# Kernel optimization log

Hardware: AMD Instinct MI355X
Metric: run time of the kernel (lower is better)

## Reference

```python
import jax, jax.numpy as jnp
import numpy as np

N_NODES = 100000
N_EDGES = 1600000
IN_F = 64
OUT_F = 40
K_HOPS = 3
N_CLUSTERS = 10000


def setup_inputs() -> dict:
    key = jax.random.key(0)
    k1, k2, k3, k4 = jax.random.split(key, 4)
    x = jax.random.normal(k1, (N_NODES, IN_F), dtype=jnp.float32)
    edge_index = jax.random.randint(k2, (2, N_EDGES), 0, N_NODES, dtype=jnp.int32)
    cluster_index = jax.random.randint(k3, (N_NODES,), 0, N_CLUSTERS, dtype=jnp.int32)
    W = jax.random.normal(k4, (OUT_F, IN_F), dtype=jnp.float32) * (1.0 / np.sqrt(IN_F))
    b = jnp.zeros((OUT_F,), dtype=jnp.float32)
    return {"x": x, "edge_index": edge_index, "cluster_index": cluster_index,
            "num_clusters": N_CLUSTERS, "W": W, "b": b}


def reference(x, edge_index, cluster_index, num_clusters, W, b):
    N = x.shape[0]
    self_loop = jnp.arange(N, dtype=edge_index.dtype)
    row = jnp.concatenate([edge_index[0], self_loop])  # target nodes
    col = jnp.concatenate([edge_index[1], self_loop])  # source nodes
    ones = jnp.ones(row.shape[0], dtype=x.dtype)
    deg = jax.ops.segment_sum(ones, row, num_segments=N)
    dinv = jax.lax.rsqrt(jnp.maximum(deg, 1.0))
    norm = dinv[row] * dinv[col]  # [E+N] symmetric GCN normalization
    # K-hop propagation: x <- D^{-1/2} (A+I) D^{-1/2} x, K times
    for _ in range(K_HOPS):
        x = jax.ops.segment_sum(x[col] * norm[:, None], row, num_segments=N)
    # cluster/compress: segment-mean of node features per cluster -> [C, F]
    cnt = jax.ops.segment_sum(jnp.ones(N, dtype=x.dtype), cluster_index,
                              num_segments=num_clusters)
    xc = jax.ops.segment_sum(x, cluster_index, num_segments=num_clusters)
    xc = xc / jnp.maximum(cnt, 1.0)[:, None]
    # dense linear on compressed rows, then reconstruct (gather back)
    h = xc @ W.T + b  # [C, OUT_F]
    out = h[cluster_index]  # [N, OUT_F]
    # original module computes log_softmax into a local `out` but returns x
    return out
```

## Files before the change

### kernel.cpp

```cpp
#include <hip/hip_runtime.h>

#define N_NODES    100000
#define N_EDGES    1600000
#define IN_F       64
#define OUT_F      40
#define N_CLUSTERS 10000

#define BUCK_SHIFT 7
#define BROWS      128
#define NBUCK      ((N_NODES + BROWS - 1) >> BUCK_SHIFT)
#define CAP        2560
#define TILE_E     4096
#define EPT        (TILE_E / 256)

typedef _Float16 half_t;
typedef _Float16 half4_t __attribute__((ext_vector_type(4)));

__global__ __launch_bounds__(256) void bin_scatter_kernel(
        const int* __restrict__ rows, const int* __restrict__ cols,
        int* __restrict__ bcursor, unsigned* __restrict__ bins) {
    __shared__ uint2 se[TILE_E];
    __shared__ int lh[NBUCK];
    __shared__ int lsc[NBUCK];
    __shared__ int lb[NBUCK];
    __shared__ int sc[256];
    int t = threadIdx.x;
    for (int i = t; i < NBUCK; i += 256) lh[i] = 0;
    __syncthreads();
    int e0 = blockIdx.x * TILE_E;
    int r[EPT], c[EPT], rk[EPT];
    #pragma unroll
    for (int k = 0; k < EPT; ++k) {
        int e = e0 + t + k * 256;
        if (e < N_EDGES) {
            r[k] = rows[e]; c[k] = cols[e];
            rk[k] = atomicAdd(&lh[r[k] >> BUCK_SHIFT], 1);
        } else r[k] = -1;
    }
    __syncthreads();
    int b4 = t * 4;
    int a0 = (b4 + 0 < NBUCK) ? lh[b4 + 0] : 0;
    int a1 = (b4 + 1 < NBUCK) ? lh[b4 + 1] : 0;
    int a2 = (b4 + 2 < NBUCK) ? lh[b4 + 2] : 0;
    int a3 = (b4 + 3 < NBUCK) ? lh[b4 + 3] : 0;
    int thr = a0 + a1 + a2 + a3;
    sc[t] = thr;
    __syncthreads();
    for (int off = 1; off < 256; off <<= 1) {
        int a = (t >= off) ? sc[t - off] : 0;
        __syncthreads();
        sc[t] += a;
        __syncthreads();
    }
    int ex = sc[t] - thr;
    if (b4 + 0 < NBUCK) { lsc[b4 + 0] = ex;                lb[b4 + 0] = a0 ? atomicAdd(&bcursor[b4 + 0], a0) : 0; }
    if (b4 + 1 < NBUCK) { lsc[b4 + 1] = ex + a0;           lb[b4 + 1] = a1 ? atomicAdd(&bcursor[b4 + 1], a1) : 0; }
    if (b4 + 2 < NBUCK) { lsc[b4 + 2] = ex + a0 + a1;      lb[b4 + 2] = a2 ? atomicAdd(&bcursor[b4 + 2], a2) : 0; }
    if (b4 + 3 < NBUCK) { lsc[b4 + 3] = ex + a0 + a1 + a2; lb[b4 + 3] = a3 ? atomicAdd(&bcursor[b4 + 3], a3) : 0; }
    __syncthreads();
    #pragma unroll
    for (int k = 0; k < EPT; ++k) {
        if (r[k] >= 0) {
            int bu = r[k] >> BUCK_SHIFT;
            se[lsc[bu] + rk[k]] = make_uint2((unsigned)r[k], (unsigned)c[k]);
        }
    }
    __syncthreads();
    #pragma unroll
    for (int k = 0; k < EPT; ++k) {
        int idx = k * 256 + t;
        if (e0 + idx < N_EDGES) {
            uint2 u = se[idx];
            int bu = (int)(u.x >> BUCK_SHIFT);
            int pos = lb[bu] + (idx - lsc[bu]);
            if (pos < CAP)
                bins[(size_t)bu * CAP + pos] = ((u.x & (BROWS - 1)) << 17) | u.y;
        }
    }
}

__global__ __launch_bounds__(256) void csr_build_kernel(
        const unsigned* __restrict__ bins, const int* __restrict__ bcnt,
        int* __restrict__ csr_col, uint2* __restrict__ rowinfo,
        float* __restrict__ dinv, const int* __restrict__ cl,
        int* __restrict__ ccnt) {
    __shared__ int lcnt[BROWS];
    __shared__ int gbeg[BROWS];
    __shared__ int sc[BROWS];
    int b = blockIdx.x, t = threadIdx.x;
    int n = min(bcnt[b], CAP);
    const unsigned* eb = bins + (size_t)b * CAP;
    if (t < BROWS) lcnt[t] = 0;
    __syncthreads();
    for (int i = t; i < n; i += 256) atomicAdd(&lcnt[eb[i] >> 17], 1);
    __syncthreads();
    int v = (t < BROWS) ? lcnt[t] : 0;
    if (t < BROWS) sc[t] = v;
    __syncthreads();
    for (int off = 1; off < BROWS; off <<= 1) {
        int a = (t >= off && t < BROWS) ? sc[t - off] : 0;
        __syncthreads();
        if (t < BROWS) sc[t] += a;
        __syncthreads();
    }
    if (t < BROWS) {
        int beg = b * CAP + sc[t] - v;
        gbeg[t] = beg;
        int grow = (b << BUCK_SHIFT) + t;
        if (grow < N_NODES) {
            rowinfo[grow] = make_uint2((unsigned)beg, (unsigned)v);
            dinv[grow] = rsqrtf((float)(v + 1));
            atomicAdd(&ccnt[cl[grow]], 1);
        }
        lcnt[t] = 0;
    }
    __syncthreads();
    for (int i = t; i < n; i += 256) {
        unsigned u = eb[i];
        int lrow = (int)(u >> 17);
        int pos = atomicAdd(&lcnt[lrow], 1);
        csr_col[gbeg[lrow] + pos] = (int)(u & 0x1FFFFu);
    }
}

__global__ __launch_bounds__(256) void prologue_kernel(
        const float4* __restrict__ x4, const float* __restrict__ W,
        const float* __restrict__ dinv, half_t* __restrict__ z0) {
    __shared__ float Ws[OUT_F * 68];
    int t = threadIdx.x;
    for (int i = t; i < OUT_F * IN_F; i += 256)
        Ws[(i >> 6) * 68 + (i & 63)] = W[i];
    __syncthreads();
    int node = blockIdx.x * 256 + t;
    if (node >= N_NODES) return;
    float4 xr[16];
    const float4* xp = x4 + (size_t)node * 16;
    #pragma unroll
    for (int k = 0; k < 16; ++k) xr[k] = xp[k];
    float d = dinv[node];
    half4_t* zp = (half4_t*)(z0 + (size_t)node * OUT_F);
    #pragma unroll
    for (int oq = 0; oq < 10; ++oq) {
        half4_t h;
        #pragma unroll
        for (int c = 0; c < 4; ++c) {
            const float4* wr = (const float4*)(Ws + (oq * 4 + c) * 68);
            float acc = 0.f;
            #pragma unroll
            for (int k = 0; k < 16; ++k) {
                float4 wv = wr[k];
                acc += xr[k].x * wv.x + xr[k].y * wv.y
                     + xr[k].z * wv.z + xr[k].w * wv.w;
            }
            h[c] = (half_t)(acc * d);
        }
        zp[oq] = h;
    }
}

template<int FINAL>
__global__ __launch_bounds__(256, 8) void hop40_kernel(
        const half_t* __restrict__ zin, half_t* __restrict__ zout,
        const uint2* __restrict__ rowinfo, const int* __restrict__ csr_col,
        const float* __restrict__ dinv, const int* __restrict__ cl,
        float* __restrict__ xc) {
    __shared__ half4_t srow[160];
    int t = threadIdx.x;
    int w = t >> 6;
    int lane = t & 63;
    int slot = lane / 10;
    int ql = lane - slot * 10;
    int slotj = (slot < 6) ? slot : 1000;
    int nb = blockIdx.x << 4;
    #pragma unroll
    for (int i = 0; i < 4; ++i) {
        int node = nb + (w << 2) + i;
        uint2 ri = rowinfo[node];
        int beg = (int)ri.x;
        int end = beg + (int)ri.y;
        float4 acc = make_float4(0.f, 0.f, 0.f, 0.f);
        if (slot == 0) {
            half4_t v = ((const half4_t*)(zin + (size_t)node * OUT_F))[ql];
            acc.x = (float)v.x; acc.y = (float)v.y; acc.z = (float)v.z; acc.w = (float)v.w;
        }
        for (int base = beg; base < end; base += 64) {
            int idx = base + lane;
            int cv = (idx < end) ? csr_col[idx] : 0;
            int lim = min(64, end - base);
            int gmax = (lim + 23) / 24;
            for (int g = 0; g < gmax; ++g) {
                int j0 = g * 24 + slotj;
                int c0 = __shfl(cv, (j0     ) & 63);
                int c1 = __shfl(cv, (j0 +  6) & 63);
                int c2 = __shfl(cv, (j0 + 12) & 63);
                int c3 = __shfl(cv, (j0 + 18) & 63);
                half4_t v0 = ((const half4_t*)(zin + (size_t)c0 * OUT_F))[ql];
                half4_t v1 = ((const half4_t*)(zin + (size_t)c1 * OUT_F))[ql];
                half4_t v2 = ((const half4_t*)(zin + (size_t)c2 * OUT_F))[ql];
                half4_t v3 = ((const half4_t*)(zin + (size_t)c3 * OUT_F))[ql];
                float m0 = (j0      < lim) ? 1.f : 0.f;
                float m1 = (j0 +  6 < lim) ? 1.f : 0.f;
                float m2 = (j0 + 12 < lim) ? 1.f : 0.f;
                float m3 = (j0 + 18 < lim) ? 1.f : 0.f;
                acc.x += m0 * (float)v0.x; acc.y += m0 * (float)v0.y;
                acc.z += m0 * (float)v0.z; acc.w += m0 * (float)v0.w;
                acc.x += m1 * (float)v1.x; acc.y += m1 * (float)v1.y;
                acc.z += m1 * (float)v1.z; acc.w += m1 * (float)v1.w;
                acc.x += m2 * (float)v2.x; acc.y += m2 * (float)v2.y;
                acc.z += m2 * (float)v2.z; acc.w += m2 * (float)v2.w;
                acc.x += m3 * (float)v3.x; acc.y += m3 * (float)v3.y;
                acc.z += m3 * (float)v3.z; acc.w += m3 * (float)v3.w;
            }
        }
        float4 t1;
        t1.x = __shfl(acc.x, (lane + 30) & 63); t1.y = __shfl(acc.y, (lane + 30) & 63);
        t1.z = __shfl(acc.z, (lane + 30) & 63); t1.w = __shfl(acc.w, (lane + 30) & 63);
        if (lane < 30) { acc.x += t1.x; acc.y += t1.y; acc.z += t1.z; acc.w += t1.w; }
        float4 t2, t3;
        t2.x = __shfl(acc.x, (lane + 10) & 63); t2.y = __shfl(acc.y, (lane + 10) & 63);
        t2.z = __shfl(acc.z, (lane + 10) & 63); t2.w = __shfl(acc.w, (lane + 10) & 63);
        t3.x = __shfl(acc.x, (lane + 20) & 63); t3.y = __shfl(acc.y, (lane + 20) & 63);
        t3.z = __shfl(acc.z, (lane + 20) & 63); t3.w = __shfl(acc.w, (lane + 20) & 63);
        if (lane < 10) {
            acc.x += t2.x + t3.x; acc.y += t2.y + t3.y;
            acc.z += t2.z + t3.z; acc.w += t2.w + t3.w;
            float d = dinv[node];
            if (FINAL) {
                float* p = xc + cl[node] * OUT_F + ql * 4;
                atomicAdd(p + 0, acc.x * d); atomicAdd(p + 1, acc.y * d);
                atomicAdd(p + 2, acc.z * d); atomicAdd(p + 3, acc.w * d);
            } else {
                float s = d * d;
                half4_t o;
                o.x = (half_t)(acc.x * s); o.y = (half_t)(acc.y * s);
                o.z = (half_t)(acc.z * s); o.w = (half_t)(acc.w * s);
                srow[((w << 2) + i) * 10 + ql] = o;
            }
        }
    }
    if (!FINAL) {
        __syncthreads();
        if (t < 160) ((half4_t*)zout)[(size_t)blockIdx.x * 160 + t] = srow[t];
    }
}

__global__ void epilogue_kernel(const float4* __restrict__ xc4, const int* __restrict__ ccnt,
                                const float4* __restrict__ b4, const int* __restrict__ cl,
                                float4* __restrict__ out4) {
    int i = blockIdx.x * 256 + threadIdx.x;
    if (i >= N_NODES * (OUT_F / 4)) return;
    int node = i / 10;
    int q = i - node * 10;
    int c = cl[node];
    float inv = 1.0f / fmaxf((float)ccnt[c], 1.0f);
    float4 v = xc4[c * 10 + q];
    float4 bb = b4[q];
    v.x = v.x * inv + bb.x; v.y = v.y * inv + bb.y;
    v.z = v.z * inv + bb.z; v.w = v.w * inv + bb.w;
    out4[i] = v;
}

extern "C" void kernel_launch(void* const* d_in, const int* in_sizes, int n_in,
                              void* d_out, int out_size, void* d_ws, size_t ws_size,
                              hipStream_t stream) {
    const float* x    = (const float*)d_in[0];
    const int*   rows = (const int*)d_in[1];
    const int*   cols = (const int*)d_in[1] + N_EDGES;
    const int*   cl   = (const int*)d_in[2];
    const float* W    = (const float*)d_in[4];
    const float* b    = (const float*)d_in[5];
    float* out = (float*)d_out;

    size_t off = 0;
    auto alloc = [&](size_t elems) -> void* {
        void* p = (char*)d_ws + off * 4;
        off += (elems + 63) & ~(size_t)63;
        return p;
    };
    int*   ccnt    = (int*)alloc(N_CLUSTERS);
    float* xc_sum  = (float*)alloc((size_t)N_CLUSTERS * OUT_F);
    int*   bcursor = (int*)alloc(NBUCK);
    size_t zero_elems = off;
    float* dinv      = (float*)alloc(N_NODES);
    uint2* rowinfo   = (uint2*)alloc((size_t)N_NODES * 2);
    int*   csr_col   = (int*)alloc((size_t)NBUCK * CAP);
    unsigned* bins   = (unsigned*)alloc((size_t)NBUCK * CAP);
    half_t* bufA     = (half_t*)alloc((size_t)N_NODES * OUT_F / 2);
    half_t* bufB     = (half_t*)alloc((size_t)N_NODES * OUT_F / 2);
    (void)ws_size; (void)in_sizes; (void)n_in; (void)out_size;

    hipMemsetAsync(d_ws, 0, zero_elems * 4, stream);

    const int TB = (N_EDGES + TILE_E - 1) / TILE_E;
    const int HB = N_NODES / 16;

    bin_scatter_kernel<<<TB, 256, 0, stream>>>(rows, cols, bcursor, bins);
    csr_build_kernel<<<NBUCK, 256, 0, stream>>>(bins, bcursor, csr_col, rowinfo,
                                                dinv, cl, ccnt);

    prologue_kernel<<<(N_NODES + 255) / 256, 256, 0, stream>>>(
        (const float4*)x, W, dinv, bufA);

    hop40_kernel<0><<<HB, 256, 0, stream>>>(bufA, bufB, rowinfo, csr_col, dinv, cl, xc_sum);
    hop40_kernel<0><<<HB, 256, 0, stream>>>(bufB, bufA, rowinfo, csr_col, dinv, cl, xc_sum);
    hop40_kernel<1><<<HB, 256, 0, stream>>>(bufA, (half_t*)nullptr, rowinfo, csr_col, dinv, cl, xc_sum);

    epilogue_kernel<<<(N_NODES * (OUT_F / 4) + 255) / 256, 256, 0, stream>>>(
        (const float4*)xc_sum, ccnt, (const float4*)b, cl, (float4*)out);
}
```

Baseline: 315.4 us.

## Split 40-wide half features into 32+8 planar buffers for 16-byte gathers

Stores the propagated half-precision features as two arrays, a 64-byte row of 32 channels and a 16-byte row of 8 channels, so each lane gathers 8 halves (16 bytes) instead of 4. Five lanes cover a neighbor row, so twelve neighbor slots run per wavefront instead of six, halving the gather iterations per 64-edge chunk. The 32-channel part is 64-byte aligned, which should cut cache-line splits from the 80-byte rows. The cost is a longer shuffle reduction with twice as many values, more register pressure, and some lanes idle (60 of 64 used).

```diff
diff --git a/kernel.cpp b/kernel.cpp
--- a/kernel.cpp
+++ b/kernel.cpp
@@ -15,6 +15,7 @@
 
 typedef _Float16 half_t;
 typedef _Float16 half4_t __attribute__((ext_vector_type(4)));
+typedef _Float16 half8_t __attribute__((ext_vector_type(8)));
 
 __global__ __launch_bounds__(256) void bin_scatter_kernel(
         const int* __restrict__ rows, const int* __restrict__ cols,
@@ -125,7 +126,8 @@
 
 __global__ __launch_bounds__(256) void prologue_kernel(
         const float4* __restrict__ x4, const float* __restrict__ W,
-        const float* __restrict__ dinv, half_t* __restrict__ z0) {
+        const float* __restrict__ dinv, half_t* __restrict__ zA,
+        half_t* __restrict__ zB) {
     __shared__ float Ws[OUT_F * 68];
     int t = threadIdx.x;
     for (int i = t; i < OUT_F * IN_F; i += 256)
@@ -138,7 +140,8 @@
     #pragma unroll
     for (int k = 0; k < 16; ++k) xr[k] = xp[k];
     float d = dinv[node];
-    half4_t* zp = (half4_t*)(z0 + (size_t)node * OUT_F);
+    half4_t* zpA = (half4_t*)(zA + (size_t)node * 32);
+    half4_t* zpB = (half4_t*)(zB + (size_t)node * 8);
     #pragma unroll
     for (int oq = 0; oq < 10; ++oq) {
         half4_t h;
@@ -154,23 +157,28 @@
             }
             h[c] = (half_t)(acc * d);
         }
-        zp[oq] = h;
+        if (oq < 8) zpA[oq] = h; else zpB[oq - 8] = h;
     }
 }
 
 template<int FINAL>
 __global__ __launch_bounds__(256, 8) void hop40_kernel(
-        const half_t* __restrict__ zin, half_t* __restrict__ zout,
+        const half_t* __restrict__ zinA, const half_t* __restrict__ zinB,
+        half_t* __restrict__ zoutA, half_t* __restrict__ zoutB,
         const uint2* __restrict__ rowinfo, const int* __restrict__ csr_col,
         const float* __restrict__ dinv, const int* __restrict__ cl,
         float* __restrict__ xc) {
-    __shared__ half4_t srow[160];
+    __shared__ half8_t srowA[64];
+    __shared__ half8_t srowB[16];
     int t = threadIdx.x;
     int w = t >> 6;
     int lane = t & 63;
-    int slot = lane / 10;
-    int ql = lane - slot * 10;
-    int slotj = (slot < 6) ? slot : 1000;
+    int slot = lane / 5;
+    int ql = lane - slot * 5;
+    int slotj = (slot < 12) ? slot : 1000;
+    const half_t* gbase = (ql < 4) ? zinA : zinB;
+    int gsh  = (ql < 4) ? 5 : 3;
+    int goff = (ql < 4) ? ql * 8 : 0;
     int nb = blockIdx.x << 4;
     #pragma unroll
     for (int i = 0; i < 4; ++i) {
@@ -178,69 +186,107 @@
         uint2 ri = rowinfo[node];
         int beg = (int)ri.x;
         int end = beg + (int)ri.y;
-        float4 acc = make_float4(0.f, 0.f, 0.f, 0.f);
+        float4 accA = make_float4(0.f, 0.f, 0.f, 0.f);
+        float4 accB = make_float4(0.f, 0.f, 0.f, 0.f);
         if (slot == 0) {
-            half4_t v = ((const half4_t*)(zin + (size_t)node * OUT_F))[ql];
-            acc.x = (float)v.x; acc.y = (float)v.y; acc.z = (float)v.z; acc.w = (float)v.w;
+            half8_t v = *(const half8_t*)(gbase + ((size_t)node << gsh) + goff);
+            accA.x = (float)v[0]; accA.y = (float)v[1];
+            accA.z = (float)v[2]; accA.w = (float)v[3];
+            accB.x = (float)v[4]; accB.y = (float)v[5];
+            accB.z = (float)v[6]; accB.w = (float)v[7];
         }
         for (int base = beg; base < end; base += 64) {
             int idx = base + lane;
             int cv = (idx < end) ? csr_col[idx] : 0;
             int lim = min(64, end - base);
-            int gmax = (lim + 23) / 24;
+            int gmax = (lim + 47) / 48;
             for (int g = 0; g < gmax; ++g) {
-                int j0 = g * 24 + slotj;
+                int j0 = g * 48 + slotj;
                 int c0 = __shfl(cv, (j0     ) & 63);
-                int c1 = __shfl(cv, (j0 +  6) & 63);
-                int c2 = __shfl(cv, (j0 + 12) & 63);
-                int c3 = __shfl(cv, (j0 + 18) & 63);
-                half4_t v0 = ((const half4_t*)(zin + (size_t)c0 * OUT_F))[ql];
-                half4_t v1 = ((const half4_t*)(zin + (size_t)c1 * OUT_F))[ql];
-                half4_t v2 = ((const half4_t*)(zin + (size_t)c2 * OUT_F))[ql];
-                half4_t v3 = ((const half4_t*)(zin + (size_t)c3 * OUT_F))[ql];
+                int c1 = __shfl(cv, (j0 + 12) & 63);
+                int c2 = __shfl(cv, (j0 + 24) & 63);
+                int c3 = __shfl(cv, (j0 + 36) & 63);
+                half8_t v0 = *(const half8_t*)(gbase + ((size_t)c0 << gsh) + goff);
+                half8_t v1 = *(const half8_t*)(gbase + ((size_t)c1 << gsh) + goff);
+                half8_t v2 = *(const half8_t*)(gbase + ((size_t)c2 << gsh) + goff);
+                half8_t v3 = *(const half8_t*)(gbase + ((size_t)c3 << gsh) + goff);
                 float m0 = (j0      < lim) ? 1.f : 0.f;
-                float m1 = (j0 +  6 < lim) ? 1.f : 0.f;
-                float m2 = (j0 + 12 < lim) ? 1.f : 0.f;
-                float m3 = (j0 + 18 < lim) ? 1.f : 0.f;
-                acc.x += m0 * (float)v0.x; acc.y += m0 * (float)v0.y;
-                acc.z += m0 * (float)v0.z; acc.w += m0 * (float)v0.w;
-                acc.x += m1 * (float)v1.x; acc.y += m1 * (float)v1.y;
-                acc.z += m1 * (float)v1.z; acc.w += m1 * (float)v1.w;
-                acc.x += m2 * (float)v2.x; acc.y += m2 * (float)v2.y;
-                acc.z += m2 * (float)v2.z; acc.w += m2 * (float)v2.w;
-                acc.x += m3 * (float)v3.x; acc.y += m3 * (float)v3.y;
-                acc.z += m3 * (float)v3.z; acc.w += m3 * (float)v3.w;
+                float m1 = (j0 + 12 < lim) ? 1.f : 0.f;
+                float m2 = (j0 + 24 < lim) ? 1.f : 0.f;
+                float m3 = (j0 + 36 < lim) ? 1.f : 0.f;
+                accA.x += m0 * (float)v0[0]; accA.y += m0 * (float)v0[1];
+                accA.z += m0 * (float)v0[2]; accA.w += m0 * (float)v0[3];
+                accB.x += m0 * (float)v0[4]; accB.y += m0 * (float)v0[5];
+                accB.z += m0 * (float)v0[6]; accB.w += m0 * (float)v0[7];
+                accA.x += m1 * (float)v1[0]; accA.y += m1 * (float)v1[1];
+                accA.z += m1 * (float)v1[2]; accA.w += m1 * (float)v1[3];
+                accB.x += m1 * (float)v1[4]; accB.y += m1 * (float)v1[5];
+                accB.z += m1 * (float)v1[6]; accB.w += m1 * (float)v1[7];
+                accA.x += m2 * (float)v2[0]; accA.y += m2 * (float)v2[1];
+                accA.z += m2 * (float)v2[2]; accA.w += m2 * (float)v2[3];
+                accB.x += m2 * (float)v2[4]; accB.y += m2 * (float)v2[5];
+                accB.z += m2 * (float)v2[6]; accB.w += m2 * (float)v2[7];
+                accA.x += m3 * (float)v3[0]; accA.y += m3 * (float)v3[1];
+                accA.z += m3 * (float)v3[2]; accA.w += m3 * (float)v3[3];
+                accB.x += m3 * (float)v3[4]; accB.y += m3 * (float)v3[5];
+                accB.z += m3 * (float)v3[6]; accB.w += m3 * (float)v3[7];
             }
         }
-        float4 t1;
-        t1.x = __shfl(acc.x, (lane + 30) & 63); t1.y = __shfl(acc.y, (lane + 30) & 63);
-        t1.z = __shfl(acc.z, (lane + 30) & 63); t1.w = __shfl(acc.w, (lane + 30) & 63);
-        if (lane < 30) { acc.x += t1.x; acc.y += t1.y; acc.z += t1.z; acc.w += t1.w; }
-        float4 t2, t3;
-        t2.x = __shfl(acc.x, (lane + 10) & 63); t2.y = __shfl(acc.y, (lane + 10) & 63);
-        t2.z = __shfl(acc.z, (lane + 10) & 63); t2.w = __shfl(acc.w, (lane + 10) & 63);
-        t3.x = __shfl(acc.x, (lane + 20) & 63); t3.y = __shfl(acc.y, (lane + 20) & 63);
-        t3.z = __shfl(acc.z, (lane + 20) & 63); t3.w = __shfl(acc.w, (lane + 20) & 63);
-        if (lane < 10) {
-            acc.x += t2.x + t3.x; acc.y += t2.y + t3.y;
-            acc.z += t2.z + t3.z; acc.w += t2.w + t3.w;
-            float d = dinv[node];
-            if (FINAL) {
-                float* p = xc + cl[node] * OUT_F + ql * 4;
-                atomicAdd(p + 0, acc.x * d); atomicAdd(p + 1, acc.y * d);
-                atomicAdd(p + 2, acc.z * d); atomicAdd(p + 3, acc.w * d);
-            } else {
-                float s = d * d;
-                half4_t o;
-                o.x = (half_t)(acc.x * s); o.y = (half_t)(acc.y * s);
-                o.z = (half_t)(acc.z * s); o.w = (half_t)(acc.w * s);
-                srow[((w << 2) + i) * 10 + ql] = o;
+        #define FOLD8(OFF, GUARD)                                            \
+        {                                                                    \
+            float r0 = __shfl(accA.x, (lane + OFF) & 63);                    \
+            float r1 = __shfl(accA.y, (lane + OFF) & 63);                    \
+            float r2 = __shfl(accA.z, (lane + OFF) & 63);                    \
+            float r3 = __shfl(accA.w, (lane + OFF) & 63);                    \
+            float r4 = __shfl(accB.x, (lane + OFF) & 63);                    \
+            float r5 = __shfl(accB.y, (lane + OFF) & 63);                    \
+            float r6 = __shfl(accB.z, (lane + OFF) & 63);                    \
+            float r7 = __shfl(accB.w, (lane + OFF) & 63);                    \
+            if (lane < GUARD) {                                              \
+                accA.x += r0; accA.y += r1; accA.z += r2; accA.w += r3;      \
+                accB.x += r4; accB.y += r5; accB.z += r6; accB.w += r7;      \
+            }                                                                \
+        }
+        FOLD8(30, 30)
+        FOLD8(15, 15)
+        {
+            float s0 = __shfl(accA.x, (lane + 5) & 63),  u0 = __shfl(accA.x, (lane + 10) & 63);
+            float s1 = __shfl(accA.y, (lane + 5) & 63),  u1 = __shfl(accA.y, (lane + 10) & 63);
+            float s2 = __shfl(accA.z, (lane + 5) & 63),  u2 = __shfl(accA.z, (lane + 10) & 63);
+            float s3 = __shfl(accA.w, (lane + 5) & 63),  u3 = __shfl(accA.w, (lane + 10) & 63);
+            float s4 = __shfl(accB.x, (lane + 5) & 63),  u4 = __shfl(accB.x, (lane + 10) & 63);
+            float s5 = __shfl(accB.y, (lane + 5) & 63),  u5 = __shfl(accB.y, (lane + 10) & 63);
+            float s6 = __shfl(accB.z, (lane + 5) & 63),  u6 = __shfl(accB.z, (lane + 10) & 63);
+            float s7 = __shfl(accB.w, (lane + 5) & 63),  u7 = __shfl(accB.w, (lane + 10) & 63);
+            if (lane < 5) {
+                accA.x += s0 + u0; accA.y += s1 + u1; accA.z += s2 + u2; accA.w += s3 + u3;
+                accB.x += s4 + u4; accB.y += s5 + u5; accB.z += s6 + u6; accB.w += s7 + u7;
+                float d = dinv[node];
+                if (FINAL) {
+                    float* p = xc + cl[node] * OUT_F + lane * 8;
+                    atomicAdd(p + 0, accA.x * d); atomicAdd(p + 1, accA.y * d);
+                    atomicAdd(p + 2, accA.z * d); atomicAdd(p + 3, accA.w * d);
+                    atomicAdd(p + 4, accB.x * d); atomicAdd(p + 5, accB.y * d);
+                    atomicAdd(p + 6, accB.z * d); atomicAdd(p + 7, accB.w * d);
+                } else {
+                    float s = d * d;
+                    half8_t o;
+                    o[0] = (half_t)(accA.x * s); o[1] = (half_t)(accA.y * s);
+                    o[2] = (half_t)(accA.z * s); o[3] = (half_t)(accA.w * s);
+                    o[4] = (half_t)(accB.x * s); o[5] = (half_t)(accB.y * s);
+                    o[6] = (half_t)(accB.z * s); o[7] = (half_t)(accB.w * s);
+                    int row = (w << 2) + i;
+                    if (lane < 4) srowA[row * 4 + lane] = o;
+                    else          srowB[row] = o;
+                }
             }
         }
+        #undef FOLD8
     }
     if (!FINAL) {
         __syncthreads();
-        if (t < 160) ((half4_t*)zout)[(size_t)blockIdx.x * 160 + t] = srow[t];
+        if (t < 64) ((half8_t*)zoutA)[(size_t)blockIdx.x * 64 + t] = srowA[t];
+        if (t < 16) ((half8_t*)zoutB)[(size_t)blockIdx.x * 16 + t] = srowB[t];
     }
 }
 
@@ -285,8 +331,10 @@
     uint2* rowinfo   = (uint2*)alloc((size_t)N_NODES * 2);
     int*   csr_col   = (int*)alloc((size_t)NBUCK * CAP);
     unsigned* bins   = (unsigned*)alloc((size_t)NBUCK * CAP);
-    half_t* bufA     = (half_t*)alloc((size_t)N_NODES * OUT_F / 2);
-    half_t* bufB     = (half_t*)alloc((size_t)N_NODES * OUT_F / 2);
+    half_t* zA0      = (half_t*)alloc((size_t)N_NODES * 16);
+    half_t* zA1      = (half_t*)alloc((size_t)N_NODES * 16);
+    half_t* zB0      = (half_t*)alloc((size_t)N_NODES * 4);
+    half_t* zB1      = (half_t*)alloc((size_t)N_NODES * 4);
     (void)ws_size; (void)in_sizes; (void)n_in; (void)out_size;
 
     hipMemsetAsync(d_ws, 0, zero_elems * 4, stream);
@@ -299,11 +347,12 @@
                                                 dinv, cl, ccnt);
 
     prologue_kernel<<<(N_NODES + 255) / 256, 256, 0, stream>>>(
-        (const float4*)x, W, dinv, bufA);
-
-    hop40_kernel<0><<<HB, 256, 0, stream>>>(bufA, bufB, rowinfo, csr_col, dinv, cl, xc_sum);
-    hop40_kernel<0><<<HB, 256, 0, stream>>>(bufB, bufA, rowinfo, csr_col, dinv, cl, xc_sum);
-    hop40_kernel<1><<<HB, 256, 0, stream>>>(bufA, (half_t*)nullptr, rowinfo, csr_col, dinv, cl, xc_sum);
+        (const float4*)x, W, dinv, zA0, zB0);
+
+    hop40_kernel<0><<<HB, 256, 0, stream>>>(zA0, zB0, zA1, zB1, rowinfo, csr_col, dinv, cl, xc_sum);
+    hop40_kernel<0><<<HB, 256, 0, stream>>>(zA1, zB1, zA0, zB0, rowinfo, csr_col, dinv, cl, xc_sum);
+    hop40_kernel<1><<<HB, 256, 0, stream>>>(zA0, zB0, (half_t*)nullptr, (half_t*)nullptr,
+                                            rowinfo, csr_col, dinv, cl, xc_sum);
 
     epilogue_kernel<<<(N_NODES * (OUT_F / 4) + 255) / 256, 256, 0, stream>>>(
         (const float4*)xc_sum, ccnt, (const float4*)b, cl, (float4*)out);
```

Measured after the change: 421.5 us. 33.6% more time.

## Replace bucketed binning CSR build with global degree count, scan, and atomic scatter

Applied to the files above, without the earlier changes.

Swaps the two-pass bucket-binning CSR construction for a classic pipeline: global atomic degree histogram, two-level prefix scan, a rowinfo/dinv pass, and an atomic-cursor scatter of column indices into an exact-size CSR array. This removes the fixed-capacity bins and their overflow truncation, as well as the intermediate bins buffer. In exchange it issues 1.6M global atomics twice, with scattered writes, and adds three more kernel launches.

```diff
diff --git a/kernel.cpp b/kernel.cpp
--- a/kernel.cpp
+++ b/kernel.cpp
@@ -6,45 +6,25 @@
 #define OUT_F      40
 #define N_CLUSTERS 10000
 
-#define BUCK_SHIFT 7
-#define BROWS      128
-#define NBUCK      ((N_NODES + BROWS - 1) >> BUCK_SHIFT)
-#define CAP        2560
-#define TILE_E     4096
-#define EPT        (TILE_E / 256)
+#define NBLK       ((N_NODES + 255) / 256)
 
 typedef _Float16 half_t;
 typedef _Float16 half4_t __attribute__((ext_vector_type(4)));
 
-__global__ __launch_bounds__(256) void bin_scatter_kernel(
-        const int* __restrict__ rows, const int* __restrict__ cols,
-        int* __restrict__ bcursor, unsigned* __restrict__ bins) {
-    __shared__ uint2 se[TILE_E];
-    __shared__ int lh[NBUCK];
-    __shared__ int lsc[NBUCK];
-    __shared__ int lb[NBUCK];
+__global__ __launch_bounds__(256) void deg_kernel(
+        const int* __restrict__ rows, int* __restrict__ deg) {
+    int i = blockIdx.x * 256 + threadIdx.x;
+    int stride = gridDim.x * 256;
+    for (; i < N_EDGES; i += stride) atomicAdd(&deg[rows[i]], 1);
+}
+
+__global__ __launch_bounds__(256) void scan_local_kernel(
+        const int* __restrict__ deg, int* __restrict__ exloc, int* __restrict__ bsum) {
     __shared__ int sc[256];
-    int t = threadIdx.x;
-    for (int i = t; i < NBUCK; i += 256) lh[i] = 0;
-    __syncthreads();
-    int e0 = blockIdx.x * TILE_E;
-    int r[EPT], c[EPT], rk[EPT];
-    #pragma unroll
-    for (int k = 0; k < EPT; ++k) {
-        int e = e0 + t + k * 256;
-        if (e < N_EDGES) {
-            r[k] = rows[e]; c[k] = cols[e];
-            rk[k] = atomicAdd(&lh[r[k] >> BUCK_SHIFT], 1);
-        } else r[k] = -1;
-    }
-    __syncthreads();
-    int b4 = t * 4;
-    int a0 = (b4 + 0 < NBUCK) ? lh[b4 + 0] : 0;
-    int a1 = (b4 + 1 < NBUCK) ? lh[b4 + 1] : 0;
-    int a2 = (b4 + 2 < NBUCK) ? lh[b4 + 2] : 0;
-    int a3 = (b4 + 3 < NBUCK) ? lh[b4 + 3] : 0;
-    int thr = a0 + a1 + a2 + a3;
-    sc[t] = thr;
+    int b = blockIdx.x, t = threadIdx.x;
+    int i = b * 256 + t;
+    int v = (i < N_NODES) ? deg[i] : 0;
+    sc[t] = v;
     __syncthreads();
     for (int off = 1; off < 256; off <<= 1) {
         int a = (t >= off) ? sc[t - off] : 0;
@@ -52,74 +32,50 @@
         sc[t] += a;
         __syncthreads();
     }
-    int ex = sc[t] - thr;
-    if (b4 + 0 < NBUCK) { lsc[b4 + 0] = ex;                lb[b4 + 0] = a0 ? atomicAdd(&bcursor[b4 + 0], a0) : 0; }
-    if (b4 + 1 < NBUCK) { lsc[b4 + 1] = ex + a0;           lb[b4 + 1] = a1 ? atomicAdd(&bcursor[b4 + 1], a1) : 0; }
-    if (b4 + 2 < NBUCK) { lsc[b4 + 2] = ex + a0 + a1;      lb[b4 + 2] = a2 ? atomicAdd(&bcursor[b4 + 2], a2) : 0; }
-    if (b4 + 3 < NBUCK) { lsc[b4 + 3] = ex + a0 + a1 + a2; lb[b4 + 3] = a3 ? atomicAdd(&bcursor[b4 + 3], a3) : 0; }
+    if (i < N_NODES) exloc[i] = sc[t] - v;
+    if (t == 255) bsum[b] = sc[255];
+}
+
+__global__ __launch_bounds__(512) void scan_block_kernel(
+        const int* __restrict__ bsum, int* __restrict__ boff) {
+    __shared__ int sc[512];
+    int t = threadIdx.x;
+    int v = (t < NBLK) ? bsum[t] : 0;
+    sc[t] = v;
     __syncthreads();
-    #pragma unroll
-    for (int k = 0; k < EPT; ++k) {
-        if (r[k] >= 0) {
-            int bu = r[k] >> BUCK_SHIFT;
-            se[lsc[bu] + rk[k]] = make_uint2((unsigned)r[k], (unsigned)c[k]);
-        }
-    }
-    __syncthreads();
-    #pragma unroll
-    for (int k = 0; k < EPT; ++k) {
-        int idx = k * 256 + t;
-        if (e0 + idx < N_EDGES) {
-            uint2 u = se[idx];
-            int bu = (int)(u.x >> BUCK_SHIFT);
-            int pos = lb[bu] + (idx - lsc[bu]);
-            if (pos < CAP)
-                bins[(size_t)bu * CAP + pos] = ((u.x & (BROWS - 1)) << 17) | u.y;
-        }
-    }
-}
-
-__global__ __launch_bounds__(256) void csr_build_kernel(
-        const unsigned* __restrict__ bins, const int* __restrict__ bcnt,
-        int* __restrict__ csr_col, uint2* __restrict__ rowinfo,
+    for (int off = 1; off < 512; off <<= 1) {
+        int a = (t >= off) ? sc[t - off] : 0;
+        __syncthreads();
+        sc[t] += a;
+        __syncthreads();
+    }
+    if (t < NBLK) boff[t] = sc[t] - v;
+}
+
+__global__ __launch_bounds__(256) void rowinfo_kernel(
+        const int* __restrict__ deg, const int* __restrict__ exloc,
+        const int* __restrict__ boff, uint2* __restrict__ rowinfo,
         float* __restrict__ dinv, const int* __restrict__ cl,
         int* __restrict__ ccnt) {
-    __shared__ int lcnt[BROWS];
-    __shared__ int gbeg[BROWS];
-    __shared__ int sc[BROWS];
-    int b = blockIdx.x, t = threadIdx.x;
-    int n = min(bcnt[b], CAP);
-    const unsigned* eb = bins + (size_t)b * CAP;
-    if (t < BROWS) lcnt[t] = 0;
-    __syncthreads();
-    for (int i = t; i < n; i += 256) atomicAdd(&lcnt[eb[i] >> 17], 1);
-    __syncthreads();
-    int v = (t < BROWS) ? lcnt[t] : 0;
-    if (t < BROWS) sc[t] = v;
-    __syncthreads();
-    for (int off = 1; off < BROWS; off <<= 1) {
-        int a = (t >= off && t < BROWS) ? sc[t - off] : 0;
-        __syncthreads();
-        if (t < BROWS) sc[t] += a;
-        __syncthreads();
-    }
-    if (t < BROWS) {
-        int beg = b * CAP + sc[t] - v;
-        gbeg[t] = beg;
-        int grow = (b << BUCK_SHIFT) + t;
-        if (grow < N_NODES) {
-            rowinfo[grow] = make_uint2((unsigned)beg, (unsigned)v);
-            dinv[grow] = rsqrtf((float)(v + 1));
-            atomicAdd(&ccnt[cl[grow]], 1);
-        }
-        lcnt[t] = 0;
-    }
-    __syncthreads();
-    for (int i = t; i < n; i += 256) {
-        unsigned u = eb[i];
-        int lrow = (int)(u >> 17);
-        int pos = atomicAdd(&lcnt[lrow], 1);
-        csr_col[gbeg[lrow] + pos] = (int)(u & 0x1FFFFu);
+    int i = blockIdx.x * 256 + threadIdx.x;
+    if (i >= N_NODES) return;
+    int d = deg[i];
+    int beg = exloc[i] + boff[i >> 8];
+    rowinfo[i] = make_uint2((unsigned)beg, (unsigned)d);
+    dinv[i] = rsqrtf((float)(d + 1));
+    atomicAdd(&ccnt[cl[i]], 1);
+}
+
+__global__ __launch_bounds__(256) void scatter_kernel(
+        const int* __restrict__ rows, const int* __restrict__ cols,
+        const uint2* __restrict__ rowinfo, int* __restrict__ cur,
+        int* __restrict__ csr_col) {
+    int i = blockIdx.x * 256 + threadIdx.x;
+    int stride = gridDim.x * 256;
+    for (; i < N_EDGES; i += stride) {
+        int r = rows[i], c = cols[i];
+        int pos = atomicAdd(&cur[r], 1);
+        csr_col[(int)rowinfo[r].x + pos] = c;
     }
 }
 
@@ -279,24 +235,28 @@
     };
     int*   ccnt    = (int*)alloc(N_CLUSTERS);
     float* xc_sum  = (float*)alloc((size_t)N_CLUSTERS * OUT_F);
-    int*   bcursor = (int*)alloc(NBUCK);
+    int*   deg     = (int*)alloc(N_NODES);
+    int*   cur     = (int*)alloc(N_NODES);
     size_t zero_elems = off;
     float* dinv      = (float*)alloc(N_NODES);
     uint2* rowinfo   = (uint2*)alloc((size_t)N_NODES * 2);
-    int*   csr_col   = (int*)alloc((size_t)NBUCK * CAP);
-    unsigned* bins   = (unsigned*)alloc((size_t)NBUCK * CAP);
+    int*   csr_col   = (int*)alloc((size_t)N_EDGES);
+    int*   exloc     = (int*)alloc(N_NODES);
+    int*   bsum      = (int*)alloc(512);
+    int*   boff      = (int*)alloc(512);
     half_t* bufA     = (half_t*)alloc((size_t)N_NODES * OUT_F / 2);
     half_t* bufB     = (half_t*)alloc((size_t)N_NODES * OUT_F / 2);
     (void)ws_size; (void)in_sizes; (void)n_in; (void)out_size;
 
     hipMemsetAsync(d_ws, 0, zero_elems * 4, stream);
 
-    const int TB = (N_EDGES + TILE_E - 1) / TILE_E;
     const int HB = N_NODES / 16;
 
-    bin_scatter_kernel<<<TB, 256, 0, stream>>>(rows, cols, bcursor, bins);
-    csr_build_kernel<<<NBUCK, 256, 0, stream>>>(bins, bcursor, csr_col, rowinfo,
-                                                dinv, cl, ccnt);
+    deg_kernel<<<2048, 256, 0, stream>>>(rows, deg);
+    scan_local_kernel<<<NBLK, 256, 0, stream>>>(deg, exloc, bsum);
+    scan_block_kernel<<<1, 512, 0, stream>>>(bsum, boff);
+    rowinfo_kernel<<<NBLK, 256, 0, stream>>>(deg, exloc, boff, rowinfo, dinv, cl, ccnt);
+    scatter_kernel<<<2048, 256, 0, stream>>>(rows, cols, rowinfo, cur, csr_col);
 
     prologue_kernel<<<(N_NODES + 255) / 256, 256, 0, stream>>>(
         (const float4*)x, W, dinv, bufA);
```

Result: slower. 425.0 us (+34.7%).
